# Kernel tuning notes

Measured on AMD Instinct MI355X. Metric: run time of the kernel, lower is better.

The kernel has to match this reference:

```python
import jax, jax.numpy as jnp
import numpy as np

H, W = 240, 320          # dim from init_kwargs
S = 48                   # hardcoded segment count
SIDX = 4                 # startIdx
EIDX = S - 10            # S - endBias
KSIZE = 5
KVALS = [0.03125, 0.03125, 0.01562, 0.03125, 0.03125,
         0.03125, 0.04406, 0.03125, 0.04406, 0.03125,
         0.0425, 0.0625, 0.14502, 0.0625, 0.0425,
         0.03125, 0.04406, 0.03125, 0.04406, 0.03125,
         0.03125, 0.03125, 0.01562, 0.03125, 0.03125]


def setup_inputs() -> dict:
    key = jax.random.key(0)
    B, N = 32, 393216
    kx, ky, kr = jax.random.split(key, 3)
    x = jax.random.randint(kx, (B, N), 0, W, dtype=jnp.int32)
    y = jax.random.randint(ky, (B, N), 0, H, dtype=jnp.int32)
    rest = jax.random.randint(kr, (B, N, 3), 0, 2, dtype=jnp.int32)  # t,p,b unused
    events = jnp.concatenate([x[..., None], y[..., None], rest], axis=-1)
    blur_kernel = jnp.array(KVALS, dtype=jnp.float32).reshape(KSIZE, KSIZE)
    return {"events": events, "blur_kernel": blur_kernel}


def _blur(h, kernel):
    # h: [B,1,S,D]; depthwise conv with the same 5x5 kernel per batch (groups=B in torch)
    k = kernel.reshape(1, 1, KSIZE, KSIZE)
    return jax.lax.conv_general_dilated(
        h, k, (1, 1), [(2, 2), (2, 2)],
        dimension_numbers=('NCHW', 'OIHW', 'NCHW'))


def _mean_curve(coord, seg, D, segLen, kernel):
    # coord: [B,usable] int32 in [0,D); seg: [usable] segment id per event
    B = coord.shape[0]
    flat = (jnp.arange(B, dtype=jnp.int32)[:, None] * (S * D)
            + seg[None, :] * D + coord)
    hist = jnp.zeros((B * S * D,), jnp.int32).at[flat.reshape(-1)].add(1)
    hist = hist.reshape(B, 1, S, D).astype(jnp.float32)
    hist = _blur(hist, kernel)[:, 0]                                  # [B,S,D]
    mean = jnp.einsum('bsd,d->bs', hist,
                      jnp.arange(D, dtype=jnp.float32)) / jnp.float32(segLen)
    start = mean[:, SIDX:SIDX + 1]
    dis_to_center = (D // 2) - start
    aligned = jnp.round(mean - start - dis_to_center).astype(jnp.int32)
    return mean, aligned


def _outlier_first(mean):
    # outlier1d (MAD-based) on each 10-wide window starting at si, flag for element 0
    idx = jnp.arange(SIDX + 1, EIDX)[:, None] + jnp.arange(10)[None, :]  # [n,10]
    win = mean[:, idx]                                                    # [B,n,10]
    med = jnp.median(win, axis=-1, keepdims=True)
    diff = jnp.abs(win - med)
    mad = jnp.median(diff, axis=-1)
    mz = 0.6745 * diff[..., 0] / mad
    return mz > 3.0                                                       # [B,n]


def _normalize(v):
    v = v.astype(jnp.float32)
    clamp = jnp.mean(v) + 3.0 * jnp.std(v, ddof=1)   # torch std is unbiased
    return jnp.clip(v, 0.0, clamp) / clamp


def _process_one(idx_rows, out_flags):
    # idx_rows: [S, segLen] flat pixel indices; out_flags: [EIDX-SIDX-1] bool
    HW = H * W
    segLen = idx_rows.shape[1]
    ones = jnp.ones((segLen,), jnp.int32)
    container = jnp.zeros((HW,), jnp.int32).at[idx_rows[SIDX]].add(ones)
    v0 = jnp.zeros((HW,), bool).at[idx_rows[SIDX]].set(True)
    v1 = jnp.ones((HW,), bool)
    conf = jnp.zeros((HW,), jnp.int32)

    def step(carry, inp):
        container, v0, v1, conf, stopped = carry
        row, is_out = inp
        active = jnp.logical_and(~stopped, ~is_out)   # 'continue' on outlier
        vnew_raw = jnp.zeros((HW,), bool).at[row].set(True)
        conf = jnp.where(active,
                         conf + (vnew_raw & v0 & v1).astype(jnp.int32), conf)
        vnew = vnew_raw | v0
        new_info = jnp.logical_xor(vnew, v0).sum().astype(jnp.float32)
        ratio = new_info / vnew.sum().astype(jnp.float32)
        small = ratio < 0.01                           # 'break' condition
        do_upd = active & (~small)
        container = jnp.where(do_upd, container.at[row].add(ones), container)
        v1 = jnp.where(do_upd, v0, v1)
        v0 = jnp.where(do_upd, vnew, v0)
        stopped = stopped | (active & small)
        return (container, v0, v1, conf, stopped), None

    carry0 = (container, v0, v1, conf, jnp.array(False))
    (container, v0, v1, conf, _), _ = jax.lax.scan(
        step, carry0, (idx_rows[SIDX + 1:EIDX], out_flags))
    return jnp.stack([_normalize(container), _normalize(conf)]).reshape(2, H, W)


def reference(events, blur_kernel):
    B, N, _ = events.shape
    segLen = N // S
    usable = segLen * S
    x = events[:, :usable, 0]
    y = events[:, :usable, 1]
    seg = (jnp.arange(usable, dtype=jnp.int32) // segLen).astype(jnp.int32)
    meanX, alignedX = _mean_curve(x, seg, W, segLen, blur_kernel)
    meanY, alignedY = _mean_curve(y, seg, H, segLen, blur_kernel)
    outl = _outlier_first(meanX) | _outlier_first(meanY)      # [B, 33]
    xx = jnp.clip(x - jnp.take(alignedX, seg, axis=1), 0, W - 1)
    yy = jnp.clip(y - jnp.take(alignedY, seg, axis=1), 0, H - 1)
    idx = (xx + W * yy).reshape(B, S, segLen)
    return jax.vmap(_process_one)(idx, outl)                  # [B,2,H,W]
```

## Files before the change

### kernel.cpp

```cpp
#include <hip/hip_runtime.h>
#include <math.h>

#define BB      32
#define NN      393216
#define SS      48
#define SEGLEN  8192
#define WW      320
#define HH      240
#define HWSZ    76800
#define NWORDS  2400
#define NSEG    34
#define NWIN    33
#define NG      16
#define HW4     19200
#define NPC     75
#define NPF     10
#define DW      38
#define NREP    4

__global__ __launch_bounds__(256) void k_hist(const int* __restrict__ ev,
                                              int* __restrict__ histX,
                                              int* __restrict__ histY,
                                              unsigned* __restrict__ packed,
                                              int use_packed) {
    int bs = blockIdx.x;
    int b = bs / SS, s = bs % SS;
    __shared__ int hx[NREP][WW];
    __shared__ int hy[NREP][HH];
    int t = threadIdx.x;
    for (int i = t; i < NREP * WW; i += 256) ((int*)hx)[i] = 0;
    for (int i = t; i < NREP * HH; i += 256) ((int*)hy)[i] = 0;
    __syncthreads();
    int rep = t & (NREP - 1);
    size_t ebase = ((size_t)b * NN + (size_t)s * SEGLEN);
    const int4* ev4 = (const int4*)(ev + ebase * 5);
    uint4* pk4 = (uint4*)(packed + ebase);
    #pragma unroll 1
    for (int it = 0; it < 8; ++it) {
        int eq = it * 256 + t;
        int q0 = eq * 5;
        int4 v0 = ev4[q0 + 0];
        int4 v1 = ev4[q0 + 1];
        int4 v2 = ev4[q0 + 2];
        int4 v3 = ev4[q0 + 3];
        int4 v4 = ev4[q0 + 4];
        atomicAdd(&hx[rep][v0.x], 1);
        atomicAdd(&hx[rep][v1.y], 1);
        atomicAdd(&hx[rep][v2.z], 1);
        atomicAdd(&hx[rep][v3.w], 1);
        atomicAdd(&hy[rep][v0.y], 1);
        atomicAdd(&hy[rep][v1.z], 1);
        atomicAdd(&hy[rep][v2.w], 1);
        atomicAdd(&hy[rep][v4.x], 1);
        if (use_packed) {
            uint4 p;
            p.x = (unsigned)v0.x | ((unsigned)v0.y << 16);
            p.y = (unsigned)v1.y | ((unsigned)v1.z << 16);
            p.z = (unsigned)v2.z | ((unsigned)v2.w << 16);
            p.w = (unsigned)v3.w | ((unsigned)v4.x << 16);
            pk4[eq] = p;
        }
    }
    __syncthreads();
    for (int i = t; i < WW; i += 256)
        histX[(size_t)bs * WW + i] = hx[0][i] + hx[1][i] + hx[2][i] + hx[3][i];
    for (int i = t; i < HH; i += 256)
        histY[(size_t)bs * HH + i] = hy[0][i] + hy[1][i] + hy[2][i] + hy[3][i];
}

__device__ double conv_mean_partial(const int* __restrict__ histB, const float* kk,
                                    int s, int D, int t) {
    double acc = 0.0;
    for (int d = t; d < D; d += 256) {
        double c = 0.0;
        #pragma unroll
        for (int i = 0; i < 5; ++i) {
            int ss = s - 2 + i;
            if (ss < 0 || ss >= SS) continue;
            const int* row = histB + (size_t)ss * D;
            #pragma unroll
            for (int j = 0; j < 5; ++j) {
                int dd = d - 2 + j;
                if ((unsigned)dd < (unsigned)D)
                    c += (double)kk[i * 5 + j] * (double)row[dd];
            }
        }
        acc += c * (double)d;
    }
    return acc;
}

__global__ __launch_bounds__(256) void k_mean(const int* __restrict__ histX,
                                              const int* __restrict__ histY,
                                              const float* __restrict__ kern,
                                              float* __restrict__ meanX,
                                              float* __restrict__ meanY) {
    int bs = blockIdx.x;
    int b = bs / SS, s = bs % SS;
    int t = threadIdx.x;
    __shared__ float kk[25];
    __shared__ double red[256];
    if (t < 25) kk[t] = kern[t];
    __syncthreads();

    double accX = conv_mean_partial(histX + (size_t)b * SS * WW, kk, s, WW, t);
    red[t] = accX;
    __syncthreads();
    for (int off = 128; off > 0; off >>= 1) {
        if (t < off) red[t] += red[t + off];
        __syncthreads();
    }
    if (t == 0) meanX[bs] = (float)(red[0] / (double)SEGLEN);
    __syncthreads();

    double accY = conv_mean_partial(histY + (size_t)b * SS * HH, kk, s, HH, t);
    red[t] = accY;
    __syncthreads();
    for (int off = 128; off > 0; off >>= 1) {
        if (t < off) red[t] += red[t + off];
        __syncthreads();
    }
    if (t == 0) meanY[bs] = (float)(red[0] / (double)SEGLEN);
}

__device__ bool outlier_win(const float* w) {
    float a[10], srt[10];
    #pragma unroll
    for (int i = 0; i < 10; ++i) { a[i] = w[i]; srt[i] = w[i]; }
    for (int i = 1; i < 10; ++i) {
        float v = srt[i]; int j = i - 1;
        while (j >= 0 && srt[j] > v) { srt[j + 1] = srt[j]; --j; }
        srt[j + 1] = v;
    }
    float med = 0.5f * (srt[4] + srt[5]);
    float d[10];
    #pragma unroll
    for (int i = 0; i < 10; ++i) d[i] = fabsf(a[i] - med);
    float d0 = d[0];
    for (int i = 1; i < 10; ++i) {
        float v = d[i]; int j = i - 1;
        while (j >= 0 && d[j] > v) { d[j + 1] = d[j]; --j; }
        d[j + 1] = v;
    }
    float mad = 0.5f * (d[4] + d[5]);
    float mz = 0.6745f * d0 / mad;
    return mz > 3.0f;
}

__global__ __launch_bounds__(64) void k_align_outl(const float* __restrict__ meanX,
                                                   const float* __restrict__ meanY,
                                                   int* __restrict__ alignedX,
                                                   int* __restrict__ alignedY,
                                                   int* __restrict__ outl) {
    int b = blockIdx.x, t = threadIdx.x;
    __shared__ float mX[SS], mY[SS];
    if (t < SS) { mX[t] = meanX[b * SS + t]; mY[t] = meanY[b * SS + t]; }
    __syncthreads();
    if (t < SS) {
        float sX = mX[4];
        float dX = (float)(WW / 2) - sX;
        alignedX[b * SS + t] = (int)rintf((mX[t] - sX) - dX);
        float sY = mY[4];
        float dY = (float)(HH / 2) - sY;
        alignedY[b * SS + t] = (int)rintf((mY[t] - sY) - dY);
    }
    if (t < NWIN) {
        int i = 5 + t;
        bool f = outlier_win(&mX[i]) || outlier_win(&mY[i]);
        outl[b * NWIN + t] = f ? 1 : 0;
    }
}

__global__ __launch_bounds__(256) void k_bitmap(const int* __restrict__ ev,
                                                const unsigned* __restrict__ packed,
                                                int use_packed,
                                                const int* __restrict__ alignedX,
                                                const int* __restrict__ alignedY,
                                                unsigned* __restrict__ bitmaps) {
    int b = blockIdx.x / NSEG;
    int si = blockIdx.x % NSEG;
    int s = 4 + si;
    __shared__ unsigned bm[NWORDS];
    for (int w = threadIdx.x; w < NWORDS; w += 256) bm[w] = 0u;
    __syncthreads();
    int ax = alignedX[b * SS + s];
    int ay = alignedY[b * SS + s];
    size_t ebase = ((size_t)b * NN + (size_t)s * SEGLEN);
    for (int i = threadIdx.x; i < SEGLEN; i += 256) {
        int x, y;
        if (use_packed) {
            unsigned p = packed[ebase + i];
            x = (int)(p & 0xFFFFu);
            y = (int)(p >> 16);
        } else {
            x = ev[(ebase + i) * 5 + 0];
            y = ev[(ebase + i) * 5 + 1];
        }
        int xx = min(max(x - ax, 0), WW - 1);
        int yy = min(max(y - ay, 0), HH - 1);
        int p = xx + WW * yy;
        atomicOr(&bm[p >> 5], 1u << (p & 31));
    }
    __syncthreads();
    unsigned* dst = bitmaps + ((size_t)b * NSEG + si) * NWORDS;
    for (int w = threadIdx.x; w < NWORDS; w += 256) dst[w] = bm[w];
}

__global__ __launch_bounds__(64) void k_decide(const unsigned* __restrict__ bitmaps,
                                               const int* __restrict__ outl,
                                               int* __restrict__ code,
                                               int* __restrict__ updFlag) {
    int b = blockIdx.x;
    int lane = threadIdx.x;
    const unsigned* base = bitmaps + (size_t)b * NSEG * NWORDS;
    unsigned v0r[DW];
    #pragma unroll
    for (int k = 0; k < DW; ++k) {
        int w = lane + (k << 6);
        v0r[k] = (w < NWORDS) ? base[w] : 0u;
    }
    if (lane < SS) updFlag[b * SS + lane] = 0;
    bool stopped = false;
    for (int s = 5; s <= 37; ++s) {
        int c = 0;
        if (!stopped && !outl[b * NWIN + (s - 5)]) {
            const unsigned* Vs = base + (size_t)(s - 4) * NWORDS;
            unsigned raw[DW];
            #pragma unroll
            for (int k = 0; k < DW; ++k) {
                int w = lane + (k << 6);
                raw[k] = (w < NWORDS) ? Vs[w] : 0u;
            }
            int ni = 0, tot = 0;
            #pragma unroll
            for (int k = 0; k < DW; ++k) {
                ni  += __popc(raw[k] & ~v0r[k]);
                tot += __popc(raw[k] | v0r[k]);
            }
            #pragma unroll
            for (int off = 1; off < 64; off <<= 1) {
                ni  += __shfl_xor(ni, off);
                tot += __shfl_xor(tot, off);
            }
            float ratio = (float)ni / (float)tot;
            if (ratio < 0.01f) {
                stopped = true;
                c = 1;
            } else {
                c = 2;
                #pragma unroll
                for (int k = 0; k < DW; ++k) v0r[k] |= raw[k];
            }
        }
        if (lane == 0) {
            code[b * NWIN + (s - 5)] = c;
            if (c == 2) updFlag[b * SS + s] = 1;
        }
    }
}

__global__ __launch_bounds__(256) void k_conf(const unsigned* __restrict__ bitmaps,
                                              const int* __restrict__ code,
                                              int* __restrict__ conf,
                                              long long* __restrict__ partF) {
    int b = blockIdx.y;
    int t = threadIdx.x;
    int w = blockIdx.x * 256 + t;
    __shared__ int sc[NWIN];
    if (t < NWIN) sc[t] = code[b * NWIN + t];
    __syncthreads();
    long long s1 = 0, s2 = 0;
    if (w < NWORDS) {
        const unsigned* base = bitmaps + (size_t)b * NSEG * NWORDS;
        unsigned v0 = base[w];
        unsigned vv = v0;
        unsigned c0 = 0, c1 = 0, c2 = 0, c3 = 0, c4 = 0, c5 = 0;
        for (int s = 5; s <= 37; ++s) {
            int cd = sc[s - 5];
            if (cd == 0) continue;
            unsigned raw = base[(size_t)(s - 4) * NWORDS + w];
            unsigned carry = raw & vv, nc;
            nc = c0 & carry; c0 ^= carry; carry = nc;
            nc = c1 & carry; c1 ^= carry; carry = nc;
            nc = c2 & carry; c2 ^= carry; carry = nc;
            nc = c3 & carry; c3 ^= carry; carry = nc;
            nc = c4 & carry; c4 ^= carry; carry = nc;
            c5 ^= carry;
            if (cd == 2) { vv = v0; v0 |= raw; }
        }
        int4* dst4 = (int4*)(conf + (size_t)b * HWSZ + (size_t)w * 32);
        #pragma unroll
        for (int j4 = 0; j4 < 8; ++j4) {
            int4 o;
            int j = j4 * 4;
            o.x = (int)((c0 >> (j+0)) & 1u) | ((int)((c1 >> (j+0)) & 1u) << 1)
                | ((int)((c2 >> (j+0)) & 1u) << 2) | ((int)((c3 >> (j+0)) & 1u) << 3)
                | ((int)((c4 >> (j+0)) & 1u) << 4) | ((int)((c5 >> (j+0)) & 1u) << 5);
            o.y = (int)((c0 >> (j+1)) & 1u) | ((int)((c1 >> (j+1)) & 1u) << 1)
                | ((int)((c2 >> (j+1)) & 1u) << 2) | ((int)((c3 >> (j+1)) & 1u) << 3)
                | ((int)((c4 >> (j+1)) & 1u) << 4) | ((int)((c5 >> (j+1)) & 1u) << 5);
            o.z = (int)((c0 >> (j+2)) & 1u) | ((int)((c1 >> (j+2)) & 1u) << 1)
                | ((int)((c2 >> (j+2)) & 1u) << 2) | ((int)((c3 >> (j+2)) & 1u) << 3)
                | ((int)((c4 >> (j+2)) & 1u) << 4) | ((int)((c5 >> (j+2)) & 1u) << 5);
            o.w = (int)((c0 >> (j+3)) & 1u) | ((int)((c1 >> (j+3)) & 1u) << 1)
                | ((int)((c2 >> (j+3)) & 1u) << 2) | ((int)((c3 >> (j+3)) & 1u) << 3)
                | ((int)((c4 >> (j+3)) & 1u) << 4) | ((int)((c5 >> (j+3)) & 1u) << 5);
            dst4[j4] = o;
            s1 += o.x + o.y + o.z + o.w;
            s2 += (long long)o.x * o.x + (long long)o.y * o.y
                + (long long)o.z * o.z + (long long)o.w * o.w;
        }
    }
    #pragma unroll
    for (int off = 32; off > 0; off >>= 1) {
        s1 += __shfl_down(s1, off);
        s2 += __shfl_down(s2, off);
    }
    __shared__ long long r1[4], r2[4];
    if ((t & 63) == 0) { r1[t >> 6] = s1; r2[t >> 6] = s2; }
    __syncthreads();
    if (t == 0) {
        long long S1 = r1[0] + r1[1] + r1[2] + r1[3];
        long long S2 = r2[0] + r2[1] + r2[2] + r2[3];
        partF[((size_t)b * NPF + blockIdx.x) * 2 + 0] = S1;
        partF[((size_t)b * NPF + blockIdx.x) * 2 + 1] = S2;
    }
}

__global__ __launch_bounds__(256) void k_hcount(const int* __restrict__ ev,
                                                const unsigned* __restrict__ packed,
                                                int use_packed,
                                                const int* __restrict__ alignedX,
                                                const int* __restrict__ alignedY,
                                                const int* __restrict__ updFlag,
                                                unsigned* __restrict__ planes) {
    int g = blockIdx.x, b = blockIdx.y;
    __shared__ unsigned hist[HW4];
    for (int i = threadIdx.x; i < HW4; i += 256) hist[i] = 0u;
    __syncthreads();
    for (int si = g; si < NSEG; si += NG) {
        int s = 4 + si;
        if (si != 0 && updFlag[b * SS + s] == 0) continue;
        int ax = alignedX[b * SS + s];
        int ay = alignedY[b * SS + s];
        size_t ebase = ((size_t)b * NN + (size_t)s * SEGLEN);
        for (int i = threadIdx.x; i < SEGLEN; i += 256) {
            int x, y;
            if (use_packed) {
                unsigned p = packed[ebase + i];
                x = (int)(p & 0xFFFFu);
                y = (int)(p >> 16);
            } else {
                x = ev[(ebase + i) * 5 + 0];
                y = ev[(ebase + i) * 5 + 1];
            }
            int xx = min(max(x - ax, 0), WW - 1);
            int yy = min(max(y - ay, 0), HH - 1);
            int p = xx + WW * yy;
            atomicAdd(&hist[p >> 2], 1u << (8 * (p & 3)));
        }
    }
    __syncthreads();
    unsigned* dst = planes + ((size_t)b * NG + g) * HW4;
    for (int i = threadIdx.x; i < HW4; i += 256) dst[i] = hist[i];
}

__global__ __launch_bounds__(256) void k_merge(const unsigned* __restrict__ planes,
                                               int* __restrict__ container,
                                               long long* __restrict__ partC) {
    int b = blockIdx.y;
    int t = threadIdx.x;
    int w = blockIdx.x * 256 + t;
    int c0 = 0, c1 = 0, c2 = 0, c3 = 0;
    #pragma unroll
    for (int g = 0; g < NG; ++g) {
        unsigned v = planes[((size_t)b * NG + g) * HW4 + w];
        c0 += (int)(v & 255u);
        c1 += (int)((v >> 8) & 255u);
        c2 += (int)((v >> 16) & 255u);
        c3 += (int)(v >> 24);
    }
    int4 o; o.x = c0; o.y = c1; o.z = c2; o.w = c3;
    ((int4*)(container + (size_t)b * HWSZ))[w] = o;
    long long s1 = c0 + c1 + c2 + c3;
    long long s2 = (long long)c0 * c0 + (long long)c1 * c1
                 + (long long)c2 * c2 + (long long)c3 * c3;
    #pragma unroll
    for (int off = 32; off > 0; off >>= 1) {
        s1 += __shfl_down(s1, off);
        s2 += __shfl_down(s2, off);
    }
    __shared__ long long r1[4], r2[4];
    if ((t & 63) == 0) { r1[t >> 6] = s1; r2[t >> 6] = s2; }
    __syncthreads();
    if (t == 0) {
        long long S1 = r1[0] + r1[1] + r1[2] + r1[3];
        long long S2 = r2[0] + r2[1] + r2[2] + r2[3];
        partC[((size_t)b * NPC + blockIdx.x) * 2 + 0] = S1;
        partC[((size_t)b * NPC + blockIdx.x) * 2 + 1] = S2;
    }
}

__global__ __launch_bounds__(64) void k_clamp(const long long* __restrict__ partC,
                                              const long long* __restrict__ partF,
                                              float* __restrict__ clamps) {
    int id = blockIdx.x;
    int b = id >> 1, arr = id & 1;
    const long long* p = arr ? (partF + (size_t)b * NPF * 2)
                             : (partC + (size_t)b * NPC * 2);
    int n = arr ? NPF : NPC;
    int t = threadIdx.x;
    long long s1 = 0, s2 = 0;
    for (int i = t; i < n; i += 64) { s1 += p[i * 2]; s2 += p[i * 2 + 1]; }
    #pragma unroll
    for (int off = 32; off > 0; off >>= 1) {
        s1 += __shfl_down(s1, off);
        s2 += __shfl_down(s2, off);
    }
    if (t == 0) {
        double nn = (double)HWSZ;
        double sum = (double)s1, sumsq = (double)s2;
        double meanv = sum / nn;
        double var = (sumsq - sum * sum / nn) / (nn - 1.0);
        if (var < 0.0) var = 0.0;
        clamps[id] = (float)(meanv + 3.0 * sqrt(var));
    }
}

__global__ __launch_bounds__(256) void k_container(const int* __restrict__ ev,
                                                   const unsigned* __restrict__ packed,
                                                   int use_packed,
                                                   const int* __restrict__ alignedX,
                                                   const int* __restrict__ alignedY,
                                                   const int* __restrict__ updFlag,
                                                   int* __restrict__ container) {
    int b = blockIdx.x / NSEG;
    int si = blockIdx.x % NSEG;
    int s = 4 + si;
    if (si != 0 && updFlag[b * SS + s] == 0) return;
    int ax = alignedX[b * SS + s];
    int ay = alignedY[b * SS + s];
    int* cb = container + (size_t)b * HWSZ;
    size_t ebase = ((size_t)b * NN + (size_t)s * SEGLEN);
    for (int i = threadIdx.x; i < SEGLEN; i += 256) {
        int x, y;
        if (use_packed) {
            unsigned p = packed[ebase + i];
            x = (int)(p & 0xFFFFu);
            y = (int)(p >> 16);
        } else {
            x = ev[(ebase + i) * 5 + 0];
            y = ev[(ebase + i) * 5 + 1];
        }
        int xx = min(max(x - ax, 0), WW - 1);
        int yy = min(max(y - ay, 0), HH - 1);
        atomicAdd(&cb[xx + WW * yy], 1);
    }
}

__global__ __launch_bounds__(256) void k_stats(const int* __restrict__ container,
                                               const int* __restrict__ conf,
                                               float* __restrict__ clamps) {
    int id = blockIdx.x;
    int b = id >> 1, arr = id & 1;
    const int* src = (arr ? conf : container) + (size_t)b * HWSZ;
    int t = threadIdx.x;
    long long s1 = 0, s2 = 0;
    for (int i = t; i < HWSZ; i += 256) {
        long long v = src[i];
        s1 += v;
        s2 += v * v;
    }
    __shared__ long long r1[256], r2[256];
    r1[t] = s1; r2[t] = s2;
    __syncthreads();
    for (int off = 128; off > 0; off >>= 1) {
        if (t < off) { r1[t] += r1[t + off]; r2[t] += r2[t + off]; }
        __syncthreads();
    }
    if (t == 0) {
        double n = (double)HWSZ;
        double sum = (double)r1[0], sumsq = (double)r2[0];
        double meanv = sum / n;
        double var = (sumsq - sum * sum / n) / (n - 1.0);
        if (var < 0.0) var = 0.0;
        clamps[id] = (float)(meanv + 3.0 * sqrt(var));
    }
}

__global__ __launch_bounds__(256) void k_out(const int* __restrict__ container,
                                             const int* __restrict__ conf,
                                             const float* __restrict__ clamps,
                                             float* __restrict__ out) {
    size_t idx4 = (size_t)blockIdx.x * 256 + threadIdx.x;
    int b   = (int)(idx4 / (2 * (HWSZ / 4)));
    int r   = (int)(idx4 % (2 * (HWSZ / 4)));
    int arr = r / (HWSZ / 4);
    int p4  = r % (HWSZ / 4);
    const int4* src = (const int4*)((arr ? conf : container) + (size_t)b * HWSZ);
    int4 v = src[p4];
    float c = clamps[b * 2 + arr];
    float4 o;
    o.x = fminf((float)v.x, c) / c;
    o.y = fminf((float)v.y, c) / c;
    o.z = fminf((float)v.z, c) / c;
    o.w = fminf((float)v.w, c) / c;
    ((float4*)out)[idx4] = o;
}

extern "C" void kernel_launch(void* const* d_in, const int* in_sizes, int n_in,
                              void* d_out, int out_size, void* d_ws, size_t ws_size,
                              hipStream_t stream) {
    const int* ev = (const int*)d_in[0];
    const float* kern = (const float*)d_in[1];
    float* out = (float*)d_out;

    char* ws = (char*)d_ws;
    size_t o = 0;
    auto alloc = [&](size_t bytes) {
        size_t r = o;
        o += (bytes + 255) & ~(size_t)255;
        return r;
    };
    int*      histX    = (int*)      (ws + alloc((size_t)BB * SS * WW * 4));
    int*      histY    = (int*)      (ws + alloc((size_t)BB * SS * HH * 4));
    float*    meanX    = (float*)    (ws + alloc((size_t)BB * SS * 4));
    float*    meanY    = (float*)    (ws + alloc((size_t)BB * SS * 4));
    int*      alignedX = (int*)      (ws + alloc((size_t)BB * SS * 4));
    int*      alignedY = (int*)      (ws + alloc((size_t)BB * SS * 4));
    int*      outl     = (int*)      (ws + alloc((size_t)BB * NWIN * 4));
    unsigned* bitmaps  = (unsigned*) (ws + alloc((size_t)BB * NSEG * NWORDS * 4));
    int*      updFlag  = (int*)      (ws + alloc((size_t)BB * SS * 4));
    int*      code     = (int*)      (ws + alloc((size_t)BB * NWIN * 4));
    float*    clamps   = (float*)    (ws + alloc((size_t)BB * 2 * 4));
    long long* partC   = (long long*)(ws + alloc((size_t)BB * NPC * 2 * 8));
    long long* partF   = (long long*)(ws + alloc((size_t)BB * NPF * 2 * 8));
    int*      container= (int*)      (ws + alloc((size_t)BB * HWSZ * 4));
    int*      conf     = (int*)      (ws + alloc((size_t)BB * HWSZ * 4));
    size_t planes_off = alloc((size_t)BB * NG * HW4 * 4);
    int use_planes = (o <= ws_size) ? 1 : 0;
    unsigned* planes = use_planes ? (unsigned*)(ws + planes_off) : (unsigned*)ws;
    size_t packed_off = alloc((size_t)BB * NN * 4);
    int use_packed = (o <= ws_size) ? 1 : 0;
    unsigned* packed = use_packed ? (unsigned*)(ws + packed_off) : (unsigned*)ws;

    k_hist      <<<BB * SS,   256, 0, stream>>>(ev, histX, histY, packed, use_packed);
    k_mean      <<<BB * SS,   256, 0, stream>>>(histX, histY, kern, meanX, meanY);
    k_align_outl<<<BB,         64, 0, stream>>>(meanX, meanY, alignedX, alignedY, outl);
    k_bitmap    <<<BB * NSEG, 256, 0, stream>>>(ev, packed, use_packed, alignedX, alignedY, bitmaps);
    k_decide    <<<BB,         64, 0, stream>>>(bitmaps, outl, code, updFlag);
    {
        dim3 grid(NPF, BB);
        k_conf  <<<grid,      256, 0, stream>>>(bitmaps, code, conf, partF);
    }
    if (use_planes) {
        dim3 g1(NG, BB);
        k_hcount<<<g1,        256, 0, stream>>>(ev, packed, use_packed, alignedX, alignedY, updFlag, planes);
        dim3 g2(NPC, BB);
        k_merge <<<g2,        256, 0, stream>>>(planes, container, partC);
        k_clamp <<<BB * 2,     64, 0, stream>>>(partC, partF, clamps);
    } else {
        hipMemsetAsync(container, 0, (size_t)BB * HWSZ * 4, stream);
        k_container<<<BB * NSEG, 256, 0, stream>>>(ev, packed, use_packed, alignedX, alignedY, updFlag, container);
        k_stats <<<BB * 2,    256, 0, stream>>>(container, conf, clamps);
    }
    k_out       <<<(BB * 2 * HWSZ) / 1024, 256, 0, stream>>>(container, conf, clamps, out);
}
```

Before: 511.2 us.

## Replace histogram+blur mean with closed-form sums and edge counts

The per-segment histograms and the 5x5 blur/mean kernel are replaced by per-segment sums of x and y plus counts of events at the two border columns on each side. The blurred weighted mean is then derived algebraically from these statistics in a small per-batch kernel. This removes the shared-memory atomics, the histogram buffers and one kernel launch. The trade-off is a more fragile closed-form expression that must reproduce the zero-padded boundary behaviour exactly.

```diff
diff --git a/kernel.cpp b/kernel.cpp
--- a/kernel.cpp
+++ b/kernel.cpp
@@ -16,25 +16,22 @@
 #define NPC     75
 #define NPF     10
 #define DW      38
-#define NREP    4
-
-__global__ __launch_bounds__(256) void k_hist(const int* __restrict__ ev,
-                                              int* __restrict__ histX,
-                                              int* __restrict__ histY,
+#define STST    16
+
+
+__global__ __launch_bounds__(256) void k_stat(const int* __restrict__ ev,
+                                              int* __restrict__ stats,
                                               unsigned* __restrict__ packed,
                                               int use_packed) {
     int bs = blockIdx.x;
     int b = bs / SS, s = bs % SS;
-    __shared__ int hx[NREP][WW];
-    __shared__ int hy[NREP][HH];
     int t = threadIdx.x;
-    for (int i = t; i < NREP * WW; i += 256) ((int*)hx)[i] = 0;
-    for (int i = t; i < NREP * HH; i += 256) ((int*)hy)[i] = 0;
-    __syncthreads();
-    int rep = t & (NREP - 1);
     size_t ebase = ((size_t)b * NN + (size_t)s * SEGLEN);
     const int4* ev4 = (const int4*)(ev + ebase * 5);
     uint4* pk4 = (uint4*)(packed + ebase);
+    int v[10];
+    #pragma unroll
+    for (int j = 0; j < 10; ++j) v[j] = 0;
     #pragma unroll 1
     for (int it = 0; it < 8; ++it) {
         int eq = it * 256 + t;
@@ -44,83 +41,44 @@
         int4 v2 = ev4[q0 + 2];
         int4 v3 = ev4[q0 + 3];
         int4 v4 = ev4[q0 + 4];
-        atomicAdd(&hx[rep][v0.x], 1);
-        atomicAdd(&hx[rep][v1.y], 1);
-        atomicAdd(&hx[rep][v2.z], 1);
-        atomicAdd(&hx[rep][v3.w], 1);
-        atomicAdd(&hy[rep][v0.y], 1);
-        atomicAdd(&hy[rep][v1.z], 1);
-        atomicAdd(&hy[rep][v2.w], 1);
-        atomicAdd(&hy[rep][v4.x], 1);
+        int xs[4] = { v0.x, v1.y, v2.z, v3.w };
+        int ys[4] = { v0.y, v1.z, v2.w, v4.x };
+        #pragma unroll
+        for (int e = 0; e < 4; ++e) {
+            int x = xs[e], y = ys[e];
+            v[0] += x;
+            v[1] += y;
+            v[2] += (x == 0);
+            v[3] += (x == 1);
+            v[4] += (x == WW - 2);
+            v[5] += (x == WW - 1);
+            v[6] += (y == 0);
+            v[7] += (y == 1);
+            v[8] += (y == HH - 2);
+            v[9] += (y == HH - 1);
+        }
         if (use_packed) {
             uint4 p;
-            p.x = (unsigned)v0.x | ((unsigned)v0.y << 16);
-            p.y = (unsigned)v1.y | ((unsigned)v1.z << 16);
-            p.z = (unsigned)v2.z | ((unsigned)v2.w << 16);
-            p.w = (unsigned)v3.w | ((unsigned)v4.x << 16);
+            p.x = (unsigned)xs[0] | ((unsigned)ys[0] << 16);
+            p.y = (unsigned)xs[1] | ((unsigned)ys[1] << 16);
+            p.z = (unsigned)xs[2] | ((unsigned)ys[2] << 16);
+            p.w = (unsigned)xs[3] | ((unsigned)ys[3] << 16);
             pk4[eq] = p;
         }
     }
-    __syncthreads();
-    for (int i = t; i < WW; i += 256)
-        histX[(size_t)bs * WW + i] = hx[0][i] + hx[1][i] + hx[2][i] + hx[3][i];
-    for (int i = t; i < HH; i += 256)
-        histY[(size_t)bs * HH + i] = hy[0][i] + hy[1][i] + hy[2][i] + hy[3][i];
-}
-
-__device__ double conv_mean_partial(const int* __restrict__ histB, const float* kk,
-                                    int s, int D, int t) {
-    double acc = 0.0;
-    for (int d = t; d < D; d += 256) {
-        double c = 0.0;
+    #pragma unroll
+    for (int off = 32; off > 0; off >>= 1) {
         #pragma unroll
-        for (int i = 0; i < 5; ++i) {
-            int ss = s - 2 + i;
-            if (ss < 0 || ss >= SS) continue;
-            const int* row = histB + (size_t)ss * D;
-            #pragma unroll
-            for (int j = 0; j < 5; ++j) {
-                int dd = d - 2 + j;
-                if ((unsigned)dd < (unsigned)D)
-                    c += (double)kk[i * 5 + j] * (double)row[dd];
-            }
-        }
-        acc += c * (double)d;
-    }
-    return acc;
-}
-
-__global__ __launch_bounds__(256) void k_mean(const int* __restrict__ histX,
-                                              const int* __restrict__ histY,
-                                              const float* __restrict__ kern,
-                                              float* __restrict__ meanX,
-                                              float* __restrict__ meanY) {
-    int bs = blockIdx.x;
-    int b = bs / SS, s = bs % SS;
-    int t = threadIdx.x;
-    __shared__ float kk[25];
-    __shared__ double red[256];
-    if (t < 25) kk[t] = kern[t];
-    __syncthreads();
-
-    double accX = conv_mean_partial(histX + (size_t)b * SS * WW, kk, s, WW, t);
-    red[t] = accX;
-    __syncthreads();
-    for (int off = 128; off > 0; off >>= 1) {
-        if (t < off) red[t] += red[t + off];
-        __syncthreads();
-    }
-    if (t == 0) meanX[bs] = (float)(red[0] / (double)SEGLEN);
-    __syncthreads();
-
-    double accY = conv_mean_partial(histY + (size_t)b * SS * HH, kk, s, HH, t);
-    red[t] = accY;
-    __syncthreads();
-    for (int off = 128; off > 0; off >>= 1) {
-        if (t < off) red[t] += red[t + off];
-        __syncthreads();
-    }
-    if (t == 0) meanY[bs] = (float)(red[0] / (double)SEGLEN);
+        for (int j = 0; j < 10; ++j) v[j] += __shfl_down(v[j], off);
+    }
+    __shared__ int red[4][10];
+    if ((t & 63) == 0) {
+        #pragma unroll
+        for (int j = 0; j < 10; ++j) red[t >> 6][j] = v[j];
+    }
+    __syncthreads();
+    if (t < 10)
+        stats[(size_t)bs * STST + t] = red[0][t] + red[1][t] + red[2][t] + red[3][t];
 }
 
 __device__ bool outlier_win(const float* w) {
@@ -147,14 +105,49 @@
     return mz > 3.0f;
 }
 
-__global__ __launch_bounds__(64) void k_align_outl(const float* __restrict__ meanX,
-                                                   const float* __restrict__ meanY,
-                                                   int* __restrict__ alignedX,
-                                                   int* __restrict__ alignedY,
-                                                   int* __restrict__ outl) {
+__device__ double mean_closed(const int* __restrict__ st, const double* kd,
+                              int s, int D) {
+    return 0.0;
+}
+
+__global__ __launch_bounds__(64) void k_meanstats(const int* __restrict__ stats,
+                                                  const float* __restrict__ kern,
+                                                  int* __restrict__ alignedX,
+                                                  int* __restrict__ alignedY,
+                                                  int* __restrict__ outl) {
     int b = blockIdx.x, t = threadIdx.x;
+    __shared__ float kk[25];
     __shared__ float mX[SS], mY[SS];
-    if (t < SS) { mX[t] = meanX[b * SS + t]; mY[t] = meanY[b * SS + t]; }
+    if (t < 25) kk[t] = kern[t];
+    __syncthreads();
+    if (t < SS) {
+        double accX = 0.0, accY = 0.0;
+        #pragma unroll
+        for (int i = 0; i < 5; ++i) {
+            int sp = t + i - 2;
+            if (sp < 0 || sp >= SS) continue;
+            double k0 = (double)kk[i * 5 + 0];
+            double k1 = (double)kk[i * 5 + 1];
+            double k2 = (double)kk[i * 5 + 2];
+            double k3 = (double)kk[i * 5 + 3];
+            double k4 = (double)kk[i * 5 + 4];
+            double Ki = k0 + k1 + k2 + k3 + k4;
+            double Mi = -2.0 * k0 - k1 + k3 + 2.0 * k4;
+            const int* st = stats + (size_t)(b * SS + sp) * STST;
+            accX += Ki * (double)st[0] + Mi * (double)SEGLEN
+                  + (double)st[2] * (2.0 * k0 + k1)
+                  + (double)st[3] * k0
+                  - (double)st[4] * (k4 * (double)WW)
+                  - (double)st[5] * (k3 * (double)WW + k4 * (double)(WW + 1));
+            accY += Ki * (double)st[1] + Mi * (double)SEGLEN
+                  + (double)st[6] * (2.0 * k0 + k1)
+                  + (double)st[7] * k0
+                  - (double)st[8] * (k4 * (double)HH)
+                  - (double)st[9] * (k3 * (double)HH + k4 * (double)(HH + 1));
+        }
+        mX[t] = (float)(accX / (double)SEGLEN);
+        mY[t] = (float)(accY / (double)SEGLEN);
+    }
     __syncthreads();
     if (t < SS) {
         float sX = mX[4];
@@ -522,10 +515,7 @@
         o += (bytes + 255) & ~(size_t)255;
         return r;
     };
-    int*      histX    = (int*)      (ws + alloc((size_t)BB * SS * WW * 4));
-    int*      histY    = (int*)      (ws + alloc((size_t)BB * SS * HH * 4));
-    float*    meanX    = (float*)    (ws + alloc((size_t)BB * SS * 4));
-    float*    meanY    = (float*)    (ws + alloc((size_t)BB * SS * 4));
+    int*      statsB   = (int*)      (ws + alloc((size_t)BB * SS * STST * 4));
     int*      alignedX = (int*)      (ws + alloc((size_t)BB * SS * 4));
     int*      alignedY = (int*)      (ws + alloc((size_t)BB * SS * 4));
     int*      outl     = (int*)      (ws + alloc((size_t)BB * NWIN * 4));
@@ -544,9 +534,8 @@
     int use_packed = (o <= ws_size) ? 1 : 0;
     unsigned* packed = use_packed ? (unsigned*)(ws + packed_off) : (unsigned*)ws;
 
-    k_hist      <<<BB * SS,   256, 0, stream>>>(ev, histX, histY, packed, use_packed);
-    k_mean      <<<BB * SS,   256, 0, stream>>>(histX, histY, kern, meanX, meanY);
-    k_align_outl<<<BB,         64, 0, stream>>>(meanX, meanY, alignedX, alignedY, outl);
+    k_stat      <<<BB * SS,   256, 0, stream>>>(ev, statsB, packed, use_packed);
+    k_meanstats <<<BB,         64, 0, stream>>>(statsB, kern, alignedX, alignedY, outl);
     k_bitmap    <<<BB * NSEG, 256, 0, stream>>>(ev, packed, use_packed, alignedX, alignedY, bitmaps);
     k_decide    <<<BB,         64, 0, stream>>>(bitmaps, outl, code, updFlag);
     {
```

New measurement: 492.2 us. -3.7%, faster.
